# Kernel tuning notes

Measured on AMD Instinct MI355X. Metric: run time of the kernel, lower is better.

The kernel has to match this reference:

```python
import jax, jax.numpy as jnp
import numpy as np

H = 4096      # hidden_dim
D = 128       # head_dim
NQ = 32       # n_q_heads = H // D
NKV = 8       # n_kv_heads (GQA)
EPS = 1e-5
ROTARY_BASE = 10000.0


def _rope(x):
    # Non-interleaved (GPT-NeoX / flash-attn) rotary over full head_dim.
    # x: [B, S, nheads, D]
    S = x.shape[1]
    half = D // 2
    inv_freq = 1.0 / (ROTARY_BASE ** (jnp.arange(0, D, 2, dtype=jnp.float32) / D))  # [D/2]
    freqs = jnp.arange(S, dtype=jnp.float32)[:, None] * inv_freq[None, :]           # [S, D/2]
    cos = jnp.cos(freqs)[None, :, None, :].astype(x.dtype)
    sin = jnp.sin(freqs)[None, :, None, :].astype(x.dtype)
    x1, x2 = x[..., :half], x[..., half:]
    return jnp.concatenate([x1 * cos - x2 * sin, x2 * cos + x1 * sin], axis=-1)


def setup_inputs() -> dict:
    key = jax.random.key(0)
    ks = jax.random.split(key, 7)
    B, S = 1, 2048
    std = 0.02
    return {
        "hidden_states": jax.random.normal(ks[0], (B, S, H), dtype=jnp.float32),
        "ln_w": jnp.ones((H,), dtype=jnp.float32),
        "ln_b": jnp.zeros((H,), dtype=jnp.float32),
        "wq": jax.random.normal(ks[1], (H, NQ * D), dtype=jnp.float32) * std,
        "wk": jax.random.normal(ks[2], (H, NKV * D), dtype=jnp.float32) * std,
        "wv": jax.random.normal(ks[3], (H, NKV * D), dtype=jnp.float32) * std,
        "wo": jax.random.normal(ks[4], (NQ * D, H), dtype=jnp.float32) * std,
    }


def reference(hidden_states, ln_w, ln_b, wq, wk, wv, wo):
    B, S, _ = hidden_states.shape
    # LayerNorm
    mu = jnp.mean(hidden_states, axis=-1, keepdims=True)
    var = jnp.mean(jnp.square(hidden_states - mu), axis=-1, keepdims=True)
    x = (hidden_states - mu) * jax.lax.rsqrt(var + EPS) * ln_w + ln_b
    # Fused QKV projection
    q = (x @ wq).reshape(B, S, NQ, D)
    k = (x @ wk).reshape(B, S, NKV, D)
    v = (x @ wv).reshape(B, S, NKV, D)
    # Rotary embedding on q and k
    q = _rope(q)
    k = _rope(k)
    # GQA: repeat kv heads
    rep = NQ // NKV
    k_r = jnp.repeat(k, rep, axis=2)  # [B, S, NQ, D]
    v_r = jnp.repeat(v, rep, axis=2)
    # Causal attention, softmax_scale = 1/sqrt(D)
    scale = 1.0 / np.sqrt(D)
    scores = jnp.einsum("bshd,bthd->bhst", q, k_r) * scale  # [B, NQ, S, S]
    causal = jnp.tril(jnp.ones((S, S), dtype=bool))
    scores = jnp.where(causal[None, None], scores, jnp.finfo(scores.dtype).min)
    p = jax.nn.softmax(scores, axis=-1)
    attn = jnp.einsum("bhst,bthd->bshd", p, v_r)  # [B, S, NQ, D]
    # Output projection (dropout p=0 in eval)
    out = attn.reshape(B, S, NQ * D) @ wo
    return out
```

## Files before the change

kernel.cpp:

```cpp
#include <hip/hip_runtime.h>
#include <hip/hip_bf16.h>

#define HDIM 4096
#define DHEAD 128
#define NQH 32
#define NKVH 8
#define SEQ 2048
#define QKVN 6144

typedef __bf16 bf16x8 __attribute__((ext_vector_type(8)));
typedef unsigned short ushort8 __attribute__((ext_vector_type(8)));
typedef float f32x4 __attribute__((ext_vector_type(4)));
typedef float f32x16 __attribute__((ext_vector_type(16)));
typedef unsigned int u32x4 __attribute__((ext_vector_type(4)));

#define WAIT_VM(N) __builtin_amdgcn_s_waitcnt(0xF70 | (N))

__device__ inline unsigned short f2bf(float f) {
    unsigned u = __float_as_uint(f);
    u += 0x7fffu + ((u >> 16) & 1u);
    return (unsigned short)(u >> 16);
}

__device__ inline unsigned cvtpk(float lo, float hi) {
    unsigned r;
    asm("v_cvt_pk_bf16_f32 %0, %1, %2" : "=v"(r) : "v"(lo), "v"(hi));
    return r;
}

__device__ inline void gload16(const void* g, void* l) {
    __builtin_amdgcn_global_load_lds(
        (const __attribute__((address_space(1))) unsigned int*)g,
        (__attribute__((address_space(3))) unsigned int*)l, 16, 0, 0);
}

__global__ void transpose_convert(const float* __restrict__ in, unsigned short* __restrict__ out,
                                  int K, int N) {
    __shared__ float tile[32][33];
    const int n0 = blockIdx.x * 32, k0 = blockIdx.y * 32;
    const int tx = threadIdx.x, ty = threadIdx.y;
    for (int r = 0; r < 32; r += 8)
        tile[ty + r][tx] = in[(size_t)(k0 + ty + r) * N + n0 + tx];
    __syncthreads();
    for (int r = 0; r < 32; r += 8)
        out[(size_t)(n0 + ty + r) * K + k0 + tx] = f2bf(tile[tx][ty + r]);
}

__global__ void transpose_v(const float* __restrict__ qkvf, unsigned short* __restrict__ vbt) {
    __shared__ float tile[32][33];
    const int s0 = blockIdx.x * 32, d0 = blockIdx.y * 32, hv = blockIdx.z;
    const int tx = threadIdx.x, ty = threadIdx.y;
    for (int r = 0; r < 32; r += 8)
        tile[ty + r][tx] = qkvf[(size_t)(s0 + ty + r) * QKVN + 5120 + hv * DHEAD + d0 + tx];
    __syncthreads();
    for (int r = 0; r < 32; r += 8)
        vbt[((size_t)hv * DHEAD + d0 + ty + r) * SEQ + s0 + tx] = f2bf(tile[tx][ty + r]);
}

__global__ __launch_bounds__(256) void layernorm_kernel(
    const float* __restrict__ hs, const float* __restrict__ w, const float* __restrict__ b,
    unsigned short* __restrict__ xb) {
    const int s = blockIdx.x;
    const float* row = hs + (size_t)s * HDIM;
    const int t = threadIdx.x;
    float vals[16];
    float sum = 0.f, sq = 0.f;
    for (int j = 0; j < 16; j++) {
        float v = row[j * 256 + t];
        vals[j] = v; sum += v; sq += v * v;
    }
    for (int off = 1; off < 64; off <<= 1) {
        sum += __shfl_xor(sum, off);
        sq  += __shfl_xor(sq, off);
    }
    __shared__ float ps[4], pq[4];
    if ((t & 63) == 0) { ps[t >> 6] = sum; pq[t >> 6] = sq; }
    __syncthreads();
    sum = ps[0] + ps[1] + ps[2] + ps[3];
    sq  = pq[0] + pq[1] + pq[2] + pq[3];
    const float mu = sum * (1.0f / HDIM);
    const float var = sq * (1.0f / HDIM) - mu * mu;
    const float rs = rsqrtf(var + 1e-5f);
    for (int j = 0; j < 16; j++) {
        int i = j * 256 + t;
        xb[(size_t)s * HDIM + i] = f2bf((vals[j] - mu) * rs * w[i] + b[i]);
    }
}

__global__ __launch_bounds__(512, 2) void gemm8p(
    const unsigned short* __restrict__ A, const unsigned short* __restrict__ Bt,
    float* __restrict__ C, int N, int lda, int Keff, int nbx,
    int gridInner, int ksliceElems, long long cSliceStride) {
    __shared__ __align__(16) unsigned short Abuf[2 * 2 * 256 * 32];
    __shared__ __align__(16) unsigned short Bbuf[2 * 2 * 256 * 32];

    const int slice = blockIdx.x / gridInner;
    const int inner = blockIdx.x % gridInner;
    const int cbx = nbx >> 3;
    const int xcd = inner & 7, k = inner >> 3;
    const int bx = xcd * cbx + (k % cbx);
    const int by = k / cbx;
    const int row0 = by * 256, col0 = bx * 256;
    A  += (size_t)slice * ksliceElems;
    Bt += (size_t)slice * ksliceElems;
    C  += (size_t)slice * cSliceStride;

    const int t = threadIdx.x, lane = t & 63, w = t >> 6;
    const int wr = w >> 2, wc = w & 3;
    const int r16 = lane & 15, kq = lane >> 4;

    const int srow = t >> 2;
    const int scsw = (t & 3) ^ ((srow >> 1) & 3);
    const unsigned short* aStage = A  + (size_t)(row0 + srow) * lda + scsw * 8;
    const unsigned short* bStage = Bt + (size_t)(col0 + srow) * lda + scsw * 8;
    const size_t half = 128 * (size_t)lda;
    const int wdst = w * 512;

    const int NT = Keff / 64;

#define STAGE(p0, ldsbuf, bufidx, kh, kt) do {                                  \
        const unsigned short* _g = (p0) + (size_t)(kt) * 64 + (kh) * 32;        \
        gload16(_g,        &ldsbuf[((bufidx) * 2 + (kh)) * 8192 + wdst]);       \
        gload16(_g + half, &ldsbuf[((bufidx) * 2 + (kh)) * 8192 + 4096 + wdst]);\
    } while (0)

#define LDA4(dst, bufidx, kh, ih) {                                             \
        _Pragma("unroll") for (int i = 0; i < 4; i++) {                         \
            int arow = wr * 128 + (ih) * 64 + i * 16 + r16;                     \
            dst[i] = *(const bf16x8*)&Abuf[((bufidx) * 2 + (kh)) * 8192 +       \
                     arow * 32 + (kq ^ ((arow >> 1) & 3)) * 8];                 \
        } }

#define LDB4(dst, bufidx, kh) {                                                 \
        _Pragma("unroll") for (int j = 0; j < 4; j++) {                         \
            int brow = wc * 64 + j * 16 + r16;                                  \
            dst[j] = *(const bf16x8*)&Bbuf[((bufidx) * 2 + (kh)) * 8192 +       \
                     brow * 32 + (kq ^ ((brow >> 1) & 3)) * 8];                 \
        } }

#define MM16(ih, av, bv) {                                                      \
        __builtin_amdgcn_s_setprio(1);                                          \
        _Pragma("unroll") for (int i = 0; i < 4; i++)                           \
            _Pragma("unroll") for (int j = 0; j < 4; j++)                       \
                acc[(ih) * 4 + i][j] = __builtin_amdgcn_mfma_f32_16x16x32_bf16( \
                    av[i], bv[j], acc[(ih) * 4 + i][j], 0, 0, 0);               \
        __builtin_amdgcn_s_setprio(0); }

    STAGE(aStage, Abuf, 0, 0, 0);
    STAGE(bStage, Bbuf, 0, 0, 0);
    STAGE(aStage, Abuf, 0, 1, 0);
    STAGE(bStage, Bbuf, 0, 1, 0);
    WAIT_VM(4);
    __builtin_amdgcn_s_barrier();

    f32x4 acc[8][4] = {};
    for (int kt = 0; kt < NT; ++kt) {
        const int cur = kt & 1, nxt = cur ^ 1;
        const bool nl = (kt + 1 < NT);
        bf16x8 a0[4], a1[4], bv[4];
        LDA4(a0, cur, 0, 0);
        LDB4(bv, cur, 0);
        if (nl) STAGE(aStage, Abuf, nxt, 0, kt + 1);
        MM16(0, a0, bv);
        LDA4(a1, cur, 0, 1);
        if (nl) STAGE(bStage, Bbuf, nxt, 0, kt + 1);
        MM16(1, a1, bv);
        if (nl) WAIT_VM(4); else WAIT_VM(0);
        __builtin_amdgcn_s_barrier();
        LDA4(a0, cur, 1, 0);
        LDB4(bv, cur, 1);
        if (nl) STAGE(aStage, Abuf, nxt, 1, kt + 1);
        MM16(0, a0, bv);
        LDA4(a1, cur, 1, 1);
        if (nl) STAGE(bStage, Bbuf, nxt, 1, kt + 1);
        MM16(1, a1, bv);
        if (nl) {
            WAIT_VM(4);
            __builtin_amdgcn_s_barrier();
        }
    }

    #pragma unroll
    for (int i = 0; i < 8; i++)
        #pragma unroll
        for (int j = 0; j < 4; j++)
            #pragma unroll
            for (int r = 0; r < 4; r++) {
                int row = row0 + wr * 128 + i * 16 + kq * 4 + r;
                int col = col0 + wc * 64 + j * 16 + r16;
                C[(size_t)row * N + col] = acc[i][j][r];
            }
#undef STAGE
#undef LDA4
#undef LDB4
#undef MM16
}

__global__ __launch_bounds__(256) void reduce_add(const float* __restrict__ a,
                                                  const float* __restrict__ b,
                                                  float* __restrict__ o, int n) {
    int i = (blockIdx.x * 256 + threadIdx.x) * 4;
    const int stride = gridDim.x * 256 * 4;
    for (; i < n; i += stride) {
        f32x4 x = *(const f32x4*)&a[i];
        f32x4 y = *(const f32x4*)&b[i];
        x += y;
        *(f32x4*)&o[i] = x;
    }
}

__global__ void rope_convert(const float* __restrict__ qkvf,
                             unsigned short* __restrict__ qb, unsigned short* __restrict__ kb) {
    const int s = blockIdx.x;
    const int head = blockIdx.y;
    const int d = threadIdx.x;
    const float SCALE = 0.08838834764831845f;
    const float NLOG = -0.14391156831212787f;
    float f = (float)s * __expf((float)d * NLOG);
    float sn, c;
    __sincosf(f, &sn, &c);
    if (head < NQH) {
        const float* src = qkvf + (size_t)s * QKVN + head * DHEAD;
        float x1 = src[d], x2 = src[d + 64];
        unsigned short* dst = qb + ((size_t)head * SEQ + s) * DHEAD;
        dst[d]      = f2bf((x1 * c - x2 * sn) * SCALE);
        dst[d + 64] = f2bf((x2 * c + x1 * sn) * SCALE);
    } else {
        const int hk = head - NQH;
        const float* src = qkvf + (size_t)s * QKVN + 4096 + hk * DHEAD;
        float x1 = src[d], x2 = src[d + 64];
        unsigned short* dst = kb + ((size_t)hk * SEQ + s) * DHEAD;
        dst[d]      = f2bf(x1 * c - x2 * sn);
        dst[d + 64] = f2bf(x2 * c + x1 * sn);
    }
}

__global__ __launch_bounds__(256, 2) void attention_kernel(
    const unsigned short* __restrict__ Q, const unsigned short* __restrict__ K,
    const unsigned short* __restrict__ Vt, unsigned short* __restrict__ O) {
    __shared__ __align__(16) unsigned short Ks[64 * 128];
    __shared__ __align__(16) unsigned short Vs[128 * 64];
    const int h = blockIdx.x & 31;
    const int p = 15 - (blockIdx.x >> 5);
    const int t = threadIdx.x, lane = t & 63, w = t >> 6;
    const int q31 = lane & 31, h2 = lane >> 5;
    const int q0w = p * 128 + w * 32;
    const int kbw = 2 * p + (w >> 1);
    const int kbmax = 2 * p + 1;
    const int hkv = h >> 2;

    bf16x8 qf[8];
    {
        const unsigned short* qrow = Q + ((size_t)h * SEQ + q0w + q31) * DHEAD + h2 * 8;
        #pragma unroll
        for (int ds = 0; ds < 8; ds++) qf[ds] = *(const bf16x8*)&qrow[ds * 16];
    }

    f32x16 oacc[4] = {};
    float m_r = -1e30f, l_r = 0.f;

    const unsigned short* Kg = K + (size_t)hkv * SEQ * DHEAD;
    const unsigned short* Vg = Vt + (size_t)hkv * DHEAD * SEQ;

    const int krow = t >> 4, kch = t & 15;
    const int vrow = t >> 3, vch = t & 7;
    ushort8 kreg[4], vreg[4];
    #pragma unroll
    for (int pp = 0; pp < 4; pp++) {
        kreg[pp] = *(const ushort8*)&Kg[(size_t)(pp * 16 + krow) * DHEAD + kch * 8];
        vreg[pp] = *(const ushort8*)&Vg[(size_t)(pp * 32 + vrow) * SEQ + vch * 8];
    }

    for (int kb = 0; kb <= kbmax; ++kb) {
        __syncthreads();
        #pragma unroll
        for (int pp = 0; pp < 4; pp++) {
            int row = pp * 16 + krow;
            *(ushort8*)&Ks[row * 128 + ((kch ^ (row & 7)) * 8)] = kreg[pp];
            int vr = pp * 32 + vrow;
            *(ushort8*)&Vs[vr * 64 + ((vch ^ (vr & 7)) * 8)] = vreg[pp];
        }
        if (kb < kbmax) {
            #pragma unroll
            for (int pp = 0; pp < 4; pp++) {
                kreg[pp] = *(const ushort8*)&Kg[(size_t)((kb + 1) * 64 + pp * 16 + krow) * DHEAD + kch * 8];
                vreg[pp] = *(const ushort8*)&Vg[(size_t)(pp * 32 + vrow) * SEQ + (kb + 1) * 64 + vch * 8];
            }
        }
        __syncthreads();
        if (kb > kbw) continue;

        f32x16 s0 = {}, s1 = {};
        #pragma unroll
        for (int ds = 0; ds < 8; ds++) {
            int r0 = q31;
            int c0 = (ds * 2 + h2) ^ (r0 & 7);
            bf16x8 kf0 = *(const bf16x8*)&Ks[r0 * 128 + c0 * 8];
            s0 = __builtin_amdgcn_mfma_f32_32x32x16_bf16(kf0, qf[ds], s0, 0, 0, 0);
            int r1 = 32 + q31;
            int c1 = (ds * 2 + h2) ^ (r1 & 7);
            bf16x8 kf1 = *(const bf16x8*)&Ks[r1 * 128 + c1 * 8];
            s1 = __builtin_amdgcn_mfma_f32_32x32x16_bf16(kf1, qf[ds], s1, 0, 0, 0);
        }
        if (kb == kbw) {
            const int qg = q0w + q31;
            #pragma unroll
            for (int r = 0; r < 16; r++) {
                int kpos = (r & 3) + 8 * (r >> 2) + 4 * h2;
                s0[r] = (kb * 64 + kpos > qg) ? -1e30f : s0[r];
                s1[r] = (kb * 64 + 32 + kpos > qg) ? -1e30f : s1[r];
            }
        }
        float pm = -1e30f;
        #pragma unroll
        for (int r = 0; r < 16; r++) pm = fmaxf(pm, fmaxf(s0[r], s1[r]));
        pm = fmaxf(pm, __shfl_xor(pm, 32));
        bool grow = pm > m_r + 8.f;
        if (__any(grow)) {
            float mn = fmaxf(m_r, pm);
            float sc = __expf(m_r - mn);
            l_r *= sc;
            float scr[16];
            #pragma unroll
            for (int r = 0; r < 16; r++) scr[r] = __shfl(sc, (r & 3) + 8 * (r >> 2) + 4 * h2);
            #pragma unroll
            for (int nt = 0; nt < 4; nt++)
                #pragma unroll
                for (int r = 0; r < 16; r++) oacc[nt][r] *= scr[r];
            m_r = mn;
        }
        float sum = 0.f;
        #pragma unroll
        for (int r = 0; r < 16; r++) {
            s0[r] = __expf(s0[r] - m_r); sum += s0[r];
            s1[r] = __expf(s1[r] - m_r); sum += s1[r];
        }
        sum += __shfl_xor(sum, 32);
        l_r += sum;
        unsigned ow0[8], ow1[8];
        #pragma unroll
        for (int a = 0; a < 4; a++) {
            ow0[a * 2 + 0] = cvtpk(s0[4 * a + 0], s0[4 * a + 1]);
            ow0[a * 2 + 1] = cvtpk(s0[4 * a + 2], s0[4 * a + 3]);
            ow1[a * 2 + 0] = cvtpk(s1[4 * a + 0], s1[4 * a + 1]);
            ow1[a * 2 + 1] = cvtpk(s1[4 * a + 2], s1[4 * a + 3]);
        }
        unsigned pw0[8], pw1[8];
        #pragma unroll
        for (int i = 0; i < 8; i++) {
            pw0[i] = __shfl_xor((int)ow0[i], 32);
            pw1[i] = __shfl_xor((int)ow1[i], 32);
        }
        bf16x8 pf[4];
        const bool lo = (h2 == 0);
        #pragma unroll
        for (int sub = 0; sub < 2; sub++) {
            int b0 = 2 * sub, b1 = 2 * sub + 1;
            u32x4 t0, t1;
            t0.x = lo ? ow0[b0 * 2 + 0] : pw0[b1 * 2 + 0];
            t0.y = lo ? ow0[b0 * 2 + 1] : pw0[b1 * 2 + 1];
            t0.z = lo ? pw0[b0 * 2 + 0] : ow0[b1 * 2 + 0];
            t0.w = lo ? pw0[b0 * 2 + 1] : ow0[b1 * 2 + 1];
            pf[sub] = __builtin_bit_cast(bf16x8, t0);
            t1.x = lo ? ow1[b0 * 2 + 0] : pw1[b1 * 2 + 0];
            t1.y = lo ? ow1[b0 * 2 + 1] : pw1[b1 * 2 + 1];
            t1.z = lo ? pw1[b0 * 2 + 0] : ow1[b1 * 2 + 0];
            t1.w = lo ? pw1[b0 * 2 + 1] : ow1[b1 * 2 + 1];
            pf[2 + sub] = __builtin_bit_cast(bf16x8, t1);
        }
        #pragma unroll
        for (int nt = 0; nt < 4; nt++) {
            int vr2 = nt * 32 + q31;
            #pragma unroll
            for (int kt16 = 0; kt16 < 4; kt16++) {
                int vc2 = (kt16 * 2 + h2) ^ (vr2 & 7);
                bf16x8 vf = *(const bf16x8*)&Vs[vr2 * 64 + vc2 * 8];
                oacc[nt] = __builtin_amdgcn_mfma_f32_32x32x16_bf16(pf[kt16], vf, oacc[nt], 0, 0, 0);
            }
        }
    }
    float inv = 1.0f / l_r;
    float invr[16];
    #pragma unroll
    for (int r = 0; r < 16; r++) invr[r] = __shfl(inv, (r & 3) + 8 * (r >> 2) + 4 * h2);
    #pragma unroll
    for (int nt = 0; nt < 4; nt++)
        #pragma unroll
        for (int r = 0; r < 16; r++) {
            int qg = q0w + (r & 3) + 8 * (r >> 2) + 4 * h2;
            O[(size_t)qg * HDIM + h * DHEAD + nt * 32 + q31] = f2bf(oacc[nt][r] * invr[r]);
        }
}

extern "C" void kernel_launch(void* const* d_in, const int* in_sizes, int n_in,
                              void* d_out, int out_size, void* d_ws, size_t ws_size,
                              hipStream_t stream) {
    const float* hs  = (const float*)d_in[0];
    const float* lnw = (const float*)d_in[1];
    const float* lnb = (const float*)d_in[2];
    const float* wq  = (const float*)d_in[3];
    const float* wk  = (const float*)d_in[4];
    const float* wv  = (const float*)d_in[5];
    const float* wo  = (const float*)d_in[6];
    float* out = (float*)d_out;

    char* ws = (char*)d_ws;
    size_t off = 0;
    auto alloc = [&](size_t bytes) {
        void* p = ws + off;
        off += (bytes + 255) & ~(size_t)255;
        return p;
    };
    unsigned short* xb   = (unsigned short*)alloc((size_t)SEQ * HDIM * 2);
    unsigned short* wqT  = (unsigned short*)alloc((size_t)HDIM * (NQH * DHEAD) * 2);
    unsigned short* wkT  = (unsigned short*)alloc((size_t)HDIM * (NKVH * DHEAD) * 2);
    unsigned short* wvT  = (unsigned short*)alloc((size_t)HDIM * (NKVH * DHEAD) * 2);
    unsigned short* woT  = (unsigned short*)alloc((size_t)(NQH * DHEAD) * HDIM * 2);
    float* qkvf          = (float*)alloc((size_t)SEQ * QKVN * 4);
    unsigned short* qbuf = (unsigned short*)alloc((size_t)NQH * SEQ * DHEAD * 2);
    unsigned short* kbuf = (unsigned short*)alloc((size_t)NKVH * SEQ * DHEAD * 2);
    unsigned short* vbt  = (unsigned short*)alloc((size_t)NKVH * DHEAD * SEQ * 2);
    unsigned short* attnb = (unsigned short*)qkvf;
    float* cpart = (float*)xb;

    dim3 tb(32, 8);
    transpose_convert<<<dim3(4096 / 32, 4096 / 32), tb, 0, stream>>>(wq, wqT, 4096, 4096);
    transpose_convert<<<dim3(1024 / 32, 4096 / 32), tb, 0, stream>>>(wk, wkT, 4096, 1024);
    transpose_convert<<<dim3(1024 / 32, 4096 / 32), tb, 0, stream>>>(wv, wvT, 4096, 1024);
    transpose_convert<<<dim3(4096 / 32, 4096 / 32), tb, 0, stream>>>(wo, woT, 4096, 4096);

    layernorm_kernel<<<SEQ, 256, 0, stream>>>(hs, lnw, lnb, xb);

    gemm8p<<<(2048 / 256) * (QKVN / 256), 512, 0, stream>>>(
        xb, wqT, qkvf, QKVN, 4096, 4096, QKVN / 256, (2048 / 256) * (QKVN / 256), 0, 0);

    rope_convert<<<dim3(SEQ, NQH + NKVH), 64, 0, stream>>>(qkvf, qbuf, kbuf);
    transpose_v<<<dim3(SEQ / 32, DHEAD / 32, NKVH), tb, 0, stream>>>(qkvf, vbt);

    attention_kernel<<<NQH * 16, 256, 0, stream>>>(qbuf, kbuf, vbt, attnb);

    gemm8p<<<2 * (2048 / 256) * (4096 / 256), 512, 0, stream>>>(
        attnb, woT, cpart, 4096, 4096, 2048, 4096 / 256,
        (2048 / 256) * (4096 / 256), 2048, (long long)2048 * 4096);
    reduce_add<<<2048, 256, 0, stream>>>(cpart, cpart + (size_t)2048 * 4096, out,
                                         2048 * 4096);
}
```

Measured before the change: 340.2 us.

## Replace split-K output projection with narrower-tile GEMM writing output directly

Measured after the change: 325.5 us. -4.3%, faster.

```diff
diff --git a/kernel.cpp b/kernel.cpp
--- a/kernel.cpp
+++ b/kernel.cpp
@@ -196,17 +196,94 @@
 #undef MM16
 }
 
-__global__ __launch_bounds__(256) void reduce_add(const float* __restrict__ a,
-                                                  const float* __restrict__ b,
-                                                  float* __restrict__ o, int n) {
-    int i = (blockIdx.x * 256 + threadIdx.x) * 4;
-    const int stride = gridDim.x * 256 * 4;
-    for (; i < n; i += stride) {
-        f32x4 x = *(const f32x4*)&a[i];
-        f32x4 y = *(const f32x4*)&b[i];
-        x += y;
-        *(f32x4*)&o[i] = x;
-    }
+__global__ __launch_bounds__(512, 2) void gemm8n(
+    const unsigned short* __restrict__ A, const unsigned short* __restrict__ Bt,
+    float* __restrict__ C, int N, int lda, int Keff, int nbx) {
+    __shared__ __align__(16) unsigned short Abuf[3][256 * 64];
+    __shared__ __align__(16) unsigned short Bbuf[3][128 * 64];
+
+    const int inner = blockIdx.x;
+    const int cbx = nbx >> 3;
+    const int xcd = inner & 7, kk = inner >> 3;
+    const int bx = xcd * cbx + (kk % cbx);
+    const int by = kk / cbx;
+    const int row0 = by * 256, col0 = bx * 128;
+
+    const int t = threadIdx.x, lane = t & 63, w = t >> 6;
+    const int wr = w >> 1, wc = w & 1;
+    const int r16 = lane & 15, kq = lane >> 4;
+
+    const int srow = t >> 3;
+    const int scsw = (t & 7) ^ (srow & 7);
+    const unsigned short* aStage = A  + (size_t)(row0 + srow) * lda + scsw * 8;
+    const unsigned short* bStage = Bt + (size_t)(col0 + srow) * lda + scsw * 8;
+    const size_t rstep = 64 * (size_t)lda;
+
+    const int NT = Keff / 64;
+
+#define NSTG_H0(bufi, kt) {                                                     \
+        gload16(aStage + (size_t)(kt) * 64,             &Abuf[bufi][0 * 4096 + w * 512]); \
+        gload16(aStage + (size_t)(kt) * 64 + rstep,     &Abuf[bufi][1 * 4096 + w * 512]); \
+        gload16(bStage + (size_t)(kt) * 64,             &Bbuf[bufi][0 * 4096 + w * 512]); }
+#define NSTG_H1(bufi, kt) {                                                     \
+        gload16(aStage + (size_t)(kt) * 64 + 2 * rstep, &Abuf[bufi][2 * 4096 + w * 512]); \
+        gload16(aStage + (size_t)(kt) * 64 + 3 * rstep, &Abuf[bufi][3 * 4096 + w * 512]); \
+        gload16(bStage + (size_t)(kt) * 64 + rstep,     &Bbuf[bufi][1 * 4096 + w * 512]); }
+
+#define NLDA(dst, bufi, kh) { _Pragma("unroll") for (int i = 0; i < 4; i++) {   \
+        int ar = wr * 64 + i * 16 + r16;                                        \
+        dst[i] = *(const bf16x8*)&Abuf[bufi][ar * 64 + (((kh) * 4 + kq) ^ (ar & 7)) * 8]; } }
+#define NLDB(dst, bufi, kh) { _Pragma("unroll") for (int j = 0; j < 4; j++) {   \
+        int br = wc * 64 + j * 16 + r16;                                        \
+        dst[j] = *(const bf16x8*)&Bbuf[bufi][br * 64 + (((kh) * 4 + kq) ^ (br & 7)) * 8]; } }
+
+#define MMN(av, bv) {                                                           \
+        __builtin_amdgcn_s_setprio(1);                                          \
+        _Pragma("unroll") for (int i = 0; i < 4; i++)                           \
+            _Pragma("unroll") for (int j = 0; j < 4; j++)                       \
+                acc[i][j] = __builtin_amdgcn_mfma_f32_16x16x32_bf16(            \
+                    av[i], bv[j], acc[i][j], 0, 0, 0);                          \
+        __builtin_amdgcn_s_setprio(0); }
+
+    NSTG_H0(0, 0); NSTG_H1(0, 0);
+    NSTG_H0(1, 1); NSTG_H1(1, 1);
+    WAIT_VM(6);
+    __builtin_amdgcn_s_barrier();
+
+    f32x4 acc[4][4] = {};
+    for (int kt = 0; kt < NT; ++kt) {
+        const int cur = kt % 3, nx2 = (kt + 2) % 3;
+        const bool pf = (kt + 2) < NT;
+        bf16x8 av[4], bv[4];
+        NLDA(av, cur, 0);
+        NLDB(bv, cur, 0);
+        if (pf) NSTG_H0(nx2, kt + 2);
+        MMN(av, bv);
+        NLDA(av, cur, 1);
+        NLDB(bv, cur, 1);
+        if (pf) NSTG_H1(nx2, kt + 2);
+        MMN(av, bv);
+        if (kt + 1 < NT) {
+            if (pf) WAIT_VM(6); else WAIT_VM(0);
+            __builtin_amdgcn_s_barrier();
+        }
+    }
+
+    #pragma unroll
+    for (int i = 0; i < 4; i++)
+        #pragma unroll
+        for (int j = 0; j < 4; j++)
+            #pragma unroll
+            for (int r = 0; r < 4; r++) {
+                int row = row0 + wr * 64 + i * 16 + kq * 4 + r;
+                int col = col0 + wc * 64 + j * 16 + r16;
+                C[(size_t)row * N + col] = acc[i][j][r];
+            }
+#undef NSTG_H0
+#undef NSTG_H1
+#undef NLDA
+#undef NLDB
+#undef MMN
 }
 
 __global__ void rope_convert(const float* __restrict__ qkvf,
@@ -421,7 +498,6 @@
     unsigned short* kbuf = (unsigned short*)alloc((size_t)NKVH * SEQ * DHEAD * 2);
     unsigned short* vbt  = (unsigned short*)alloc((size_t)NKVH * DHEAD * SEQ * 2);
     unsigned short* attnb = (unsigned short*)qkvf;
-    float* cpart = (float*)xb;
 
     dim3 tb(32, 8);
     transpose_convert<<<dim3(4096 / 32, 4096 / 32), tb, 0, stream>>>(wq, wqT, 4096, 4096);
@@ -439,9 +515,6 @@
 
     attention_kernel<<<NQH * 16, 256, 0, stream>>>(qbuf, kbuf, vbt, attnb);
 
-    gemm8p<<<2 * (2048 / 256) * (4096 / 256), 512, 0, stream>>>(
-        attnb, woT, cpart, 4096, 4096, 2048, 4096 / 256,
-        (2048 / 256) * (4096 / 256), 2048, (long long)2048 * 4096);
-    reduce_add<<<2048, 256, 0, stream>>>(cpart, cpart + (size_t)2048 * 4096, out,
-                                         2048 * 4096);
-}
+    gemm8n<<<(2048 / 256) * (4096 / 128), 512, 0, stream>>>(
+        attnb, woT, out, 4096, 4096, 4096, 4096 / 128);
+}
```

## Use triple-buffered K=32 GEMM pipeline and drop split-K for output projection

Applied to the files above, without the earlier changes.

Result: slower. 356.7 us (+4.9%).

```diff
diff --git a/kernel.cpp b/kernel.cpp
--- a/kernel.cpp
+++ b/kernel.cpp
@@ -15,6 +15,12 @@
 typedef unsigned int u32x4 __attribute__((ext_vector_type(4)));
 
 #define WAIT_VM(N) __builtin_amdgcn_s_waitcnt(0xF70 | (N))
+
+#define SYNC_LGKM() do {                                      \
+        __builtin_amdgcn_s_barrier();                         \
+        asm volatile("s_waitcnt lgkmcnt(0)" ::: "memory");    \
+        __builtin_amdgcn_sched_barrier(0);                    \
+    } while (0)
 
 __device__ inline unsigned short f2bf(float f) {
     unsigned u = __float_as_uint(f);
@@ -87,23 +93,18 @@
     }
 }
 
-__global__ __launch_bounds__(512, 2) void gemm8p(
+__global__ __launch_bounds__(512, 1) void gemm9(
     const unsigned short* __restrict__ A, const unsigned short* __restrict__ Bt,
-    float* __restrict__ C, int N, int lda, int Keff, int nbx,
-    int gridInner, int ksliceElems, long long cSliceStride) {
-    __shared__ __align__(16) unsigned short Abuf[2 * 2 * 256 * 32];
-    __shared__ __align__(16) unsigned short Bbuf[2 * 2 * 256 * 32];
-
-    const int slice = blockIdx.x / gridInner;
-    const int inner = blockIdx.x % gridInner;
+    float* __restrict__ C, int N, int lda, int Keff, int nbx) {
+    __shared__ __align__(16) unsigned short Abuf[3][256 * 32];
+    __shared__ __align__(16) unsigned short Bbuf[3][256 * 32];
+
+    const int inner = blockIdx.x;
     const int cbx = nbx >> 3;
-    const int xcd = inner & 7, k = inner >> 3;
-    const int bx = xcd * cbx + (k % cbx);
-    const int by = k / cbx;
+    const int xcd = inner & 7, kk = inner >> 3;
+    const int bx = xcd * cbx + (kk % cbx);
+    const int by = kk / cbx;
     const int row0 = by * 256, col0 = bx * 256;
-    A  += (size_t)slice * ksliceElems;
-    Bt += (size_t)slice * ksliceElems;
-    C  += (size_t)slice * cSliceStride;
 
     const int t = threadIdx.x, lane = t & 63, w = t >> 6;
     const int wr = w >> 2, wc = w & 3;
@@ -111,73 +112,52 @@
 
     const int srow = t >> 2;
     const int scsw = (t & 3) ^ ((srow >> 1) & 3);
-    const unsigned short* aStage = A  + (size_t)(row0 + srow) * lda + scsw * 8;
-    const unsigned short* bStage = Bt + (size_t)(col0 + srow) * lda + scsw * 8;
-    const size_t half = 128 * (size_t)lda;
+    const unsigned short* aS = A  + (size_t)(row0 + srow) * lda + scsw * 8;
+    const unsigned short* bS = Bt + (size_t)(col0 + srow) * lda + scsw * 8;
+    const size_t h128 = 128 * (size_t)lda;
     const int wdst = w * 512;
 
-    const int NT = Keff / 64;
-
-#define STAGE(p0, ldsbuf, bufidx, kh, kt) do {                                  \
-        const unsigned short* _g = (p0) + (size_t)(kt) * 64 + (kh) * 32;        \
-        gload16(_g,        &ldsbuf[((bufidx) * 2 + (kh)) * 8192 + wdst]);       \
-        gload16(_g + half, &ldsbuf[((bufidx) * 2 + (kh)) * 8192 + 4096 + wdst]);\
-    } while (0)
-
-#define LDA4(dst, bufidx, kh, ih) {                                             \
-        _Pragma("unroll") for (int i = 0; i < 4; i++) {                         \
-            int arow = wr * 128 + (ih) * 64 + i * 16 + r16;                     \
-            dst[i] = *(const bf16x8*)&Abuf[((bufidx) * 2 + (kh)) * 8192 +       \
-                     arow * 32 + (kq ^ ((arow >> 1) & 3)) * 8];                 \
-        } }
-
-#define LDB4(dst, bufidx, kh) {                                                 \
-        _Pragma("unroll") for (int j = 0; j < 4; j++) {                         \
-            int brow = wc * 64 + j * 16 + r16;                                  \
-            dst[j] = *(const bf16x8*)&Bbuf[((bufidx) * 2 + (kh)) * 8192 +       \
-                     brow * 32 + (kq ^ ((brow >> 1) & 3)) * 8];                 \
-        } }
-
-#define MM16(ih, av, bv) {                                                      \
-        __builtin_amdgcn_s_setprio(1);                                          \
-        _Pragma("unroll") for (int i = 0; i < 4; i++)                           \
-            _Pragma("unroll") for (int j = 0; j < 4; j++)                       \
-                acc[(ih) * 4 + i][j] = __builtin_amdgcn_mfma_f32_16x16x32_bf16( \
-                    av[i], bv[j], acc[(ih) * 4 + i][j], 0, 0, 0);               \
+    const int NT = Keff / 32;
+
+#define SA9(bufi, kt) { gload16(aS + (size_t)(kt) * 32,        &Abuf[bufi][wdst]); \
+                        gload16(aS + (size_t)(kt) * 32 + h128, &Abuf[bufi][4096 + wdst]); }
+#define SB9(bufi, kt) { gload16(bS + (size_t)(kt) * 32,        &Bbuf[bufi][wdst]); \
+                        gload16(bS + (size_t)(kt) * 32 + h128, &Bbuf[bufi][4096 + wdst]); }
+#define RA9(dst, bufi, ih) { _Pragma("unroll") for (int i = 0; i < 4; i++) {       \
+        int ar = wr * 128 + (ih) * 64 + i * 16 + r16;                              \
+        dst[i] = *(const bf16x8*)&Abuf[bufi][ar * 32 + (kq ^ ((ar >> 1) & 3)) * 8]; } }
+#define RB9(dst, bufi) { _Pragma("unroll") for (int j = 0; j < 4; j++) {           \
+        int br = wc * 64 + j * 16 + r16;                                           \
+        dst[j] = *(const bf16x8*)&Bbuf[bufi][br * 32 + (kq ^ ((br >> 1) & 3)) * 8]; } }
+#define MM9(ih, av, bv) { __builtin_amdgcn_s_setprio(1);                           \
+        _Pragma("unroll") for (int i = 0; i < 4; i++)                              \
+            _Pragma("unroll") for (int j = 0; j < 4; j++)                          \
+                acc[(ih) * 4 + i][j] = __builtin_amdgcn_mfma_f32_16x16x32_bf16(    \
+                    av[i], bv[j], acc[(ih) * 4 + i][j], 0, 0, 0);                  \
         __builtin_amdgcn_s_setprio(0); }
 
-    STAGE(aStage, Abuf, 0, 0, 0);
-    STAGE(bStage, Bbuf, 0, 0, 0);
-    STAGE(aStage, Abuf, 0, 1, 0);
-    STAGE(bStage, Bbuf, 0, 1, 0);
+    SA9(0, 0); SB9(0, 0);
+    SA9(1, 1); SB9(1, 1);
     WAIT_VM(4);
     __builtin_amdgcn_s_barrier();
 
     f32x4 acc[8][4] = {};
     for (int kt = 0; kt < NT; ++kt) {
-        const int cur = kt & 1, nxt = cur ^ 1;
-        const bool nl = (kt + 1 < NT);
+        const int cur = kt % 3, nx2 = (kt + 2) % 3;
+        const bool pf = (kt + 2) < NT;
         bf16x8 a0[4], a1[4], bv[4];
-        LDA4(a0, cur, 0, 0);
-        LDB4(bv, cur, 0);
-        if (nl) STAGE(aStage, Abuf, nxt, 0, kt + 1);
-        MM16(0, a0, bv);
-        LDA4(a1, cur, 0, 1);
-        if (nl) STAGE(bStage, Bbuf, nxt, 0, kt + 1);
-        MM16(1, a1, bv);
-        if (nl) WAIT_VM(4); else WAIT_VM(0);
+        RA9(a0, cur, 0);
+        RB9(bv, cur);
+        if (pf) SA9(nx2, kt + 2);
+        SYNC_LGKM();
+        MM9(0, a0, bv);
         __builtin_amdgcn_s_barrier();
-        LDA4(a0, cur, 1, 0);
-        LDB4(bv, cur, 1);
-        if (nl) STAGE(aStage, Abuf, nxt, 1, kt + 1);
-        MM16(0, a0, bv);
-        LDA4(a1, cur, 1, 1);
-        if (nl) STAGE(bStage, Bbuf, nxt, 1, kt + 1);
-        MM16(1, a1, bv);
-        if (nl) {
-            WAIT_VM(4);
-            __builtin_amdgcn_s_barrier();
-        }
+        RA9(a1, cur, 1);
+        if (pf) SB9(nx2, kt + 2);
+        SYNC_LGKM();
+        MM9(1, a1, bv);
+        if (pf) WAIT_VM(4); else WAIT_VM(0);
+        __builtin_amdgcn_s_barrier();
     }
 
     #pragma unroll
@@ -190,23 +170,89 @@
                 int col = col0 + wc * 64 + j * 16 + r16;
                 C[(size_t)row * N + col] = acc[i][j][r];
             }
-#undef STAGE
-#undef LDA4
-#undef LDB4
-#undef MM16
-}
-
-__global__ __launch_bounds__(256) void reduce_add(const float* __restrict__ a,
-                                                  const float* __restrict__ b,
-                                                  float* __restrict__ o, int n) {
-    int i = (blockIdx.x * 256 + threadIdx.x) * 4;
-    const int stride = gridDim.x * 256 * 4;
-    for (; i < n; i += stride) {
-        f32x4 x = *(const f32x4*)&a[i];
-        f32x4 y = *(const f32x4*)&b[i];
-        x += y;
-        *(f32x4*)&o[i] = x;
-    }
+#undef SA9
+#undef SB9
+#undef RA9
+#undef RB9
+#undef MM9
+}
+
+__global__ __launch_bounds__(512, 2) void gemm9n(
+    const unsigned short* __restrict__ A, const unsigned short* __restrict__ Bt,
+    float* __restrict__ C, int N, int lda, int Keff, int nbx) {
+    __shared__ __align__(16) unsigned short Abuf[3][256 * 32];
+    __shared__ __align__(16) unsigned short Bbuf[3][128 * 32];
+
+    const int inner = blockIdx.x;
+    const int cbx = nbx >> 3;
+    const int xcd = inner & 7, kk = inner >> 3;
+    const int bx = xcd * cbx + (kk % cbx);
+    const int by = kk / cbx;
+    const int row0 = by * 256, col0 = bx * 128;
+
+    const int t = threadIdx.x, lane = t & 63, w = t >> 6;
+    const int wr = w >> 1, wc = w & 1;
+    const int r16 = lane & 15, kq = lane >> 4;
+
+    const int srow = t >> 2;
+    const int scsw = (t & 3) ^ ((srow >> 1) & 3);
+    const unsigned short* aS = A  + (size_t)(row0 + srow) * lda + scsw * 8;
+    const unsigned short* bS = Bt + (size_t)(col0 + srow) * lda + scsw * 8;
+    const size_t h128 = 128 * (size_t)lda;
+    const int wdst = w * 512;
+
+    const int NT = Keff / 32;
+
+#define SAN(bufi, kt) { gload16(aS + (size_t)(kt) * 32,        &Abuf[bufi][wdst]); \
+                        gload16(aS + (size_t)(kt) * 32 + h128, &Abuf[bufi][4096 + wdst]); }
+#define SBN(bufi, kt) { gload16(bS + (size_t)(kt) * 32,        &Bbuf[bufi][wdst]); }
+#define RAN(dst, bufi) { _Pragma("unroll") for (int i = 0; i < 4; i++) {           \
+        int ar = wr * 64 + i * 16 + r16;                                           \
+        dst[i] = *(const bf16x8*)&Abuf[bufi][ar * 32 + (kq ^ ((ar >> 1) & 3)) * 8]; } }
+#define RBN(dst, bufi) { _Pragma("unroll") for (int j = 0; j < 4; j++) {           \
+        int br = wc * 64 + j * 16 + r16;                                           \
+        dst[j] = *(const bf16x8*)&Bbuf[bufi][br * 32 + (kq ^ ((br >> 1) & 3)) * 8]; } }
+#define MMN9(av, bv) { __builtin_amdgcn_s_setprio(1);                              \
+        _Pragma("unroll") for (int i = 0; i < 4; i++)                              \
+            _Pragma("unroll") for (int j = 0; j < 4; j++)                          \
+                acc[i][j] = __builtin_amdgcn_mfma_f32_16x16x32_bf16(               \
+                    av[i], bv[j], acc[i][j], 0, 0, 0);                             \
+        __builtin_amdgcn_s_setprio(0); }
+
+    SAN(0, 0); SBN(0, 0);
+    SAN(1, 1); SBN(1, 1);
+    WAIT_VM(3);
+    __builtin_amdgcn_s_barrier();
+
+    f32x4 acc[4][4] = {};
+    for (int kt = 0; kt < NT; ++kt) {
+        const int cur = kt % 3, nx2 = (kt + 2) % 3;
+        const bool pf = (kt + 2) < NT;
+        bf16x8 av[4], bv[4];
+        RAN(av, cur);
+        RBN(bv, cur);
+        if (pf) { SAN(nx2, kt + 2); SBN(nx2, kt + 2); }
+        SYNC_LGKM();
+        MMN9(av, bv);
+        if (pf) WAIT_VM(3); else WAIT_VM(0);
+        __builtin_amdgcn_s_barrier();
+    }
+
+    #pragma unroll
+    for (int i = 0; i < 4; i++)
+        #pragma unroll
+        for (int j = 0; j < 4; j++)
+            #pragma unroll
+            for (int r = 0; r < 4; r++) {
+                int row = row0 + wr * 64 + i * 16 + kq * 4 + r;
+                int col = col0 + wc * 64 + j * 16 + r16;
+                C[(size_t)row * N + col] = acc[i][j][r];
+            }
+#undef SAN
+#undef SBN
+#undef RAN
+#undef RBN
+#undef MMN9
 }
 
 __global__ void rope_convert(const float* __restrict__ qkvf,
@@ -421,7 +467,6 @@
     unsigned short* kbuf = (unsigned short*)alloc((size_t)NKVH * SEQ * DHEAD * 2);
     unsigned short* vbt  = (unsigned short*)alloc((size_t)NKVH * DHEAD * SEQ * 2);
     unsigned short* attnb = (unsigned short*)qkvf;
-    float* cpart = (float*)xb;
 
     dim3 tb(32, 8);
     transpose_convert<<<dim3(4096 / 32, 4096 / 32), tb, 0, stream>>>(wq, wqT, 4096, 4096);
@@ -431,17 +476,14 @@
 
     layernorm_kernel<<<SEQ, 256, 0, stream>>>(hs, lnw, lnb, xb);
 
-    gemm8p<<<(2048 / 256) * (QKVN / 256), 512, 0, stream>>>(
-        xb, wqT, qkvf, QKVN, 4096, 4096, QKVN / 256, (2048 / 256) * (QKVN / 256), 0, 0);
+    gemm9<<<(2048 / 256) * (QKVN / 256), 512, 0, stream>>>(
+        xb, wqT, qkvf, QKVN, 4096, 4096, QKVN / 256);
 
     rope_convert<<<dim3(SEQ, NQH + NKVH), 64, 0, stream>>>(qkvf, qbuf, kbuf);
     transpose_v<<<dim3(SEQ / 32, DHEAD / 32, NKVH), tb, 0, stream>>>(qkvf, vbt);
 
     attention_kernel<<<NQH * 16, 256, 0, stream>>>(qbuf, kbuf, vbt, attnb);
 
-    gemm8p<<<2 * (2048 / 256) * (4096 / 256), 512, 0, stream>>>(
-        attnb, woT, cpart, 4096, 4096, 2048, 4096 / 256,
-        (2048 / 256) * (4096 / 256), 2048, (long long)2048 * 4096);
-    reduce_add<<<2048, 256, 0, stream>>>(cpart, cpart + (size_t)2048 * 4096, out,
-                                         2048 * 4096);
-}
+    gemm9n<<<(2048 / 256) * (4096 / 128), 512, 0, stream>>>(
+        attnb, woT, out, 4096, 4096, 4096, 4096 / 128);
+}
```
